# Kernel tuning notes

Measured on AMD Instinct MI355X. Metric: run time of the kernel, lower is better.

Reference implementation:

```python
import jax, jax.numpy as jnp
import numpy as np

IN_F = 4096
OUT_F = 4096
NNZ = 1638400
TOKENS = 8192


def setup_inputs() -> dict:
    key = jax.random.key(0)
    k1, k2, k3, k4, k5 = jax.random.split(key, 5)
    x = jax.random.normal(k1, (TOKENS, IN_F), dtype=jnp.float32)
    weight_pruned = jax.random.normal(k2, (NNZ,), dtype=jnp.float32)
    bias = jax.random.normal(k3, (OUT_F,), dtype=jnp.float32)
    row_idx = jax.random.randint(k4, (NNZ,), 0, OUT_F, dtype=jnp.int32)
    col_idx = jax.random.randint(k5, (NNZ,), 0, IN_F, dtype=jnp.int32)
    return {"x": x, "weight_pruned": weight_pruned, "bias": bias,
            "row_idx": row_idx, "col_idx": col_idx}


def reference(x, weight_pruned, bias, row_idx, col_idx):
    # matching torch advanced-index assignment), then dense linear.
    W = jnp.zeros((OUT_F, IN_F), dtype=weight_pruned.dtype)
    W = W.at[row_idx, col_idx].set(weight_pruned)
    return x @ W.T + bias
```

## Files before the change

### kernel.cpp

```cpp
#include <hip/hip_runtime.h>
#include <hip/hip_bf16.h>
#include <cstdint>

#define TOKENS 8192
#define IN_F 4096
#define OUT_F 4096

typedef __bf16 bf16x8 __attribute__((ext_vector_type(8)));
typedef float f32x4 __attribute__((ext_vector_type(4)));

__global__ void scatter_max_kernel(const int* __restrict__ row,
                                   const int* __restrict__ col,
                                   int* __restrict__ M, int nnz) {
    int i = blockIdx.x * blockDim.x + threadIdx.x;
    if (i < nnz) {
        atomicMax(&M[(size_t)row[i] * IN_F + col[i]], i);
    }
}

__global__ void extract_convert_kernel(const int* __restrict__ M,
                                       const float* __restrict__ w,
                                       __bf16* __restrict__ Wb,
                                       const float* __restrict__ x,
                                       __bf16* __restrict__ xb,
                                       int eb) {
    if ((int)blockIdx.x < eb) {
        size_t base = ((size_t)blockIdx.x * 256 + threadIdx.x) * 8;
        int4 m0 = *(const int4*)(M + base);
        int4 m1 = *(const int4*)(M + base + 4);
        int idx[8] = {m0.x, m0.y, m0.z, m0.w, m1.x, m1.y, m1.z, m1.w};
        bf16x8 o;
#pragma unroll
        for (int j = 0; j < 8; ++j) {
            o[j] = (idx[j] >= 0) ? (__bf16)w[idx[j]] : (__bf16)0.0f;
        }
        *(bf16x8*)(Wb + base) = o;
    } else {
        size_t base = ((size_t)(blockIdx.x - eb) * 256 + threadIdx.x) * 8;
        float4 v0 = *(const float4*)(x + base);
        float4 v1 = *(const float4*)(x + base + 4);
        bf16x8 o;
        o[0] = (__bf16)v0.x; o[1] = (__bf16)v0.y;
        o[2] = (__bf16)v0.z; o[3] = (__bf16)v0.w;
        o[4] = (__bf16)v1.x; o[5] = (__bf16)v1.y;
        o[6] = (__bf16)v1.z; o[7] = (__bf16)v1.w;
        *(bf16x8*)(xb + base) = o;
    }
}

#define BK 64
#define NT (IN_F / BK)

__global__ __launch_bounds__(512, 2) void gemm256_kernel(
    const __bf16* __restrict__ A,
    const __bf16* __restrict__ B,
    const float* __restrict__ bias,
    float* __restrict__ C) {
    extern __shared__ __bf16 sm[];

    const int tid = threadIdx.x;
    const int l   = tid & 63;
    const int wid = tid >> 6;
    const int wm  = wid >> 2;
    const int wn  = wid & 3;

    const int bid = blockIdx.y * 16 + blockIdx.x;
    const int swz = (bid & 7) * 64 + (bid >> 3);
    const int n0 = (swz & 15) * 256;
    const int m0 = (swz >> 4) * 256;

    const int srow   = tid >> 3;
    const int schunk = (tid & 7) ^ (srow & 7);
    const __bf16* gA = A + (size_t)(m0 + srow) * IN_F + schunk * 8;
    const __bf16* gB = B + (size_t)(n0 + srow) * IN_F + schunk * 8;
    const int ldsw = wid * 512;

#define GLD(SRC, LEL)                                                          \
    __builtin_amdgcn_global_load_lds(                                          \
        (unsigned int __attribute__((address_space(1)))*)(SRC),                \
        (unsigned int __attribute__((address_space(3)))*)(sm + (LEL)), 16, 0, 0);

#define STAGE_A(BUF, KT) {                                                     \
    GLD(gA + (KT),              (BUF)*16384 + 0     + ldsw)                    \
    GLD(gA + 64*IN_F  + (KT),   (BUF)*16384 + 4096  + ldsw)                    \
    GLD(gA + 128*IN_F + (KT),   (BUF)*16384 + 8192  + ldsw)                    \
    GLD(gA + 192*IN_F + (KT),   (BUF)*16384 + 12288 + ldsw) }

#define STAGE_B(BUF, KT) {                                                     \
    GLD(gB + (KT),              32768 + (BUF)*16384 + 0     + ldsw)            \
    GLD(gB + 64*IN_F  + (KT),   32768 + (BUF)*16384 + 4096  + ldsw)            \
    GLD(gB + 128*IN_F + (KT),   32768 + (BUF)*16384 + 8192  + ldsw)            \
    GLD(gB + 192*IN_F + (KT),   32768 + (BUF)*16384 + 12288 + ldsw) }

    const int g    = l >> 4;
    const int fr   = l & 15;
    const int ch0  = g ^ (l & 7);
    const int ch1  = ch0 ^ 4;
    const int arow = (wm * 128 + fr) * 64;
    const int brow = (wn * 64 + fr) * 64;

    f32x4 acc[8][4] = {};
    bf16x8 a[4][2], b[2][2];

#define LDA_H(BUF, MH) {                                                                  \
    _Pragma("unroll") for (int mf = 0; mf < 4; ++mf) {                                    \
        a[mf][0] = *(const bf16x8*)(sm + (BUF)*16384 + (MH)*4096 + arow + mf*1024 + ch0*8); \
        a[mf][1] = *(const bf16x8*)(sm + (BUF)*16384 + (MH)*4096 + arow + mf*1024 + ch1*8); } }

#define LDB_P(BUF, NB) {                                                                  \
    _Pragma("unroll") for (int j = 0; j < 2; ++j) {                                       \
        b[j][0] = *(const bf16x8*)(sm + 32768 + (BUF)*16384 + brow + ((NB)+j)*1024 + ch0*8); \
        b[j][1] = *(const bf16x8*)(sm + 32768 + (BUF)*16384 + brow + ((NB)+j)*1024 + ch1*8); } }

#define MMA(MH, NB) {                                                          \
    __builtin_amdgcn_s_setprio(1);                                             \
    _Pragma("unroll") for (int mf = 0; mf < 4; ++mf)                           \
    _Pragma("unroll") for (int j = 0; j < 2; ++j) {                            \
        acc[(MH)*4+mf][(NB)+j] = __builtin_amdgcn_mfma_f32_16x16x32_bf16(      \
            a[mf][0], b[j][0], acc[(MH)*4+mf][(NB)+j], 0, 0, 0);               \
        acc[(MH)*4+mf][(NB)+j] = __builtin_amdgcn_mfma_f32_16x16x32_bf16(      \
            a[mf][1], b[j][1], acc[(MH)*4+mf][(NB)+j], 0, 0, 0); }             \
    __builtin_amdgcn_s_setprio(0); }

#define BARRIER() { asm volatile("" ::: "memory");                             \
                    __builtin_amdgcn_s_barrier();                              \
                    asm volatile("" ::: "memory"); }
#define LGKM0()   asm volatile("s_waitcnt lgkmcnt(0)" ::: "memory");
#define VMC(N)    asm volatile("s_waitcnt vmcnt(" #N ")" ::: "memory");

    STAGE_A(0, 0)
    STAGE_B(0, 0)
    STAGE_A(1, BK)
    VMC(4)
    BARRIER()

#pragma unroll 1
    for (int t = 0; t < NT; t += 2) {
        const int k1 = (t + 1) * BK;
        const int k2 = ((t + 2) & (NT - 1)) * BK;
        const int k3 = ((t + 3) & (NT - 1)) * BK;

        LDA_H(0, 0) LDB_P(0, 0) STAGE_B(1, k1)
        BARRIER() LGKM0() MMA(0, 0) BARRIER()
        LDB_P(0, 2)
        BARRIER() LGKM0() MMA(0, 2) BARRIER()
        LDA_H(0, 1)
        BARRIER() LGKM0() MMA(1, 2) BARRIER()
        LDB_P(0, 0) STAGE_A(0, k2)
        BARRIER() LGKM0() MMA(1, 0) VMC(4) BARRIER()

        LDA_H(1, 0) LDB_P(1, 0) STAGE_B(0, k2)
        BARRIER() LGKM0() MMA(0, 0) BARRIER()
        LDB_P(1, 2)
        BARRIER() LGKM0() MMA(0, 2) BARRIER()
        LDA_H(1, 1)
        BARRIER() LGKM0() MMA(1, 2) BARRIER()
        LDB_P(1, 0) STAGE_A(1, k3)
        BARRIER() LGKM0() MMA(1, 0) VMC(4) BARRIER()
    }
    VMC(0)

    float bv[4];
#pragma unroll
    for (int nf = 0; nf < 4; ++nf) bv[nf] = bias[n0 + wn * 64 + nf * 16 + fr];
    const int r0 = m0 + wm * 128 + g * 4;
#pragma unroll
    for (int mh = 0; mh < 2; ++mh)
#pragma unroll
        for (int mf = 0; mf < 4; ++mf)
#pragma unroll
            for (int nf = 0; nf < 4; ++nf) {
                const int col = n0 + wn * 64 + nf * 16 + fr;
#pragma unroll
                for (int i = 0; i < 4; ++i)
                    C[(size_t)(r0 + mh * 64 + mf * 16 + i) * OUT_F + col] =
                        acc[mh * 4 + mf][nf][i] + bv[nf];
            }
}

extern "C" void kernel_launch(void* const* d_in, const int* in_sizes, int n_in,
                              void* d_out, int out_size, void* d_ws, size_t ws_size,
                              hipStream_t stream) {
    const float* x    = (const float*)d_in[0];
    const float* w    = (const float*)d_in[1];
    const float* bias = (const float*)d_in[2];
    const int*   row  = (const int*)d_in[3];
    const int*   col  = (const int*)d_in[4];
    float* out = (float*)d_out;
    const int nnz = in_sizes[3];

    __bf16* xb = (__bf16*)d_ws;
    __bf16* Wb = (__bf16*)((char*)d_ws + (size_t)TOKENS * IN_F * 2);
    int* M = (int*)d_out;

    static bool attr_done = false;
    if (!attr_done) {
        hipFuncSetAttribute(reinterpret_cast<const void*>(gemm256_kernel),
                            hipFuncAttributeMaxDynamicSharedMemorySize, 131072);
        attr_done = true;
    }

    hipMemsetAsync(M, 0xFF, (size_t)OUT_F * IN_F * 4, stream);

    scatter_max_kernel<<<(nnz + 255) / 256, 256, 0, stream>>>(row, col, M, nnz);

    const int eb = OUT_F * IN_F / (256 * 8);
    const int cb = TOKENS * IN_F / (256 * 8);
    extract_convert_kernel<<<eb + cb, 256, 0, stream>>>(M, w, Wb, x, xb, eb);

    dim3 grid(OUT_F / 256, TOKENS / 256);
    gemm256_kernel<<<grid, 512, 131072, stream>>>(xb, Wb, bias, out);
}
```

Baseline: 567.2 us.

## Software-pipeline LDS fragment loads across MFMA phases with partial lgkm waits

Restructures the GEMM main loop so LDS fragment loads for the next phase (and the next k-tile) are issued before the current MFMA block. Each phase then waits with lgkmcnt(6) instead of fully draining, and the extra barrier pairs are gone. Separate double-buffered register sets (aP/aQ, b01E/b01O, b23) carry fragments across phases, and global stage loads are rescheduled with a single vmcnt(0) per tile. Launch bounds drop to one block per CU to make room for the extra registers, giving up occupancy in exchange for overlapping LDS reads with matrix work.

```diff
diff --git a/kernel.cpp b/kernel.cpp
--- a/kernel.cpp
+++ b/kernel.cpp
@@ -51,7 +51,7 @@
 #define BK 64
 #define NT (IN_F / BK)
 
-__global__ __launch_bounds__(512, 2) void gemm256_kernel(
+__global__ __launch_bounds__(512, 1) void gemm256_kernel(
     const __bf16* __restrict__ A,
     const __bf16* __restrict__ B,
     const float* __restrict__ bias,
@@ -100,65 +100,71 @@
     const int brow = (wn * 64 + fr) * 64;
 
     f32x4 acc[8][4] = {};
-    bf16x8 a[4][2], b[2][2];
-
-#define LDA_H(BUF, MH) {                                                                  \
-    _Pragma("unroll") for (int mf = 0; mf < 4; ++mf) {                                    \
-        a[mf][0] = *(const bf16x8*)(sm + (BUF)*16384 + (MH)*4096 + arow + mf*1024 + ch0*8); \
-        a[mf][1] = *(const bf16x8*)(sm + (BUF)*16384 + (MH)*4096 + arow + mf*1024 + ch1*8); } }
-
-#define LDB_P(BUF, NB) {                                                                  \
-    _Pragma("unroll") for (int j = 0; j < 2; ++j) {                                       \
-        b[j][0] = *(const bf16x8*)(sm + 32768 + (BUF)*16384 + brow + ((NB)+j)*1024 + ch0*8); \
-        b[j][1] = *(const bf16x8*)(sm + 32768 + (BUF)*16384 + brow + ((NB)+j)*1024 + ch1*8); } }
-
-#define MMA(MH, NB) {                                                          \
+    bf16x8 aP[4][2], aQ[4][2], b01E[2][2], b01O[2][2], b23[2][2];
+
+#define LDAF(DST, MF, BUF, MH) {                                                             \
+    DST[MF][0] = *(const bf16x8*)(sm + (BUF)*16384 + (MH)*4096 + arow + (MF)*1024 + ch0*8);  \
+    DST[MF][1] = *(const bf16x8*)(sm + (BUF)*16384 + (MH)*4096 + arow + (MF)*1024 + ch1*8); }
+
+#define LDBF(DST, J, BUF, NB) {                                                                    \
+    DST[J][0] = *(const bf16x8*)(sm + 32768 + (BUF)*16384 + brow + ((NB)+(J))*1024 + ch0*8);       \
+    DST[J][1] = *(const bf16x8*)(sm + 32768 + (BUF)*16384 + brow + ((NB)+(J))*1024 + ch1*8); }
+
+#define MMAC(AR, BR, MB, NB) {                                                 \
     __builtin_amdgcn_s_setprio(1);                                             \
     _Pragma("unroll") for (int mf = 0; mf < 4; ++mf)                           \
     _Pragma("unroll") for (int j = 0; j < 2; ++j) {                            \
-        acc[(MH)*4+mf][(NB)+j] = __builtin_amdgcn_mfma_f32_16x16x32_bf16(      \
-            a[mf][0], b[j][0], acc[(MH)*4+mf][(NB)+j], 0, 0, 0);               \
-        acc[(MH)*4+mf][(NB)+j] = __builtin_amdgcn_mfma_f32_16x16x32_bf16(      \
-            a[mf][1], b[j][1], acc[(MH)*4+mf][(NB)+j], 0, 0, 0); }             \
+        acc[(MB)+mf][(NB)+j] = __builtin_amdgcn_mfma_f32_16x16x32_bf16(        \
+            AR[mf][0], BR[j][0], acc[(MB)+mf][(NB)+j], 0, 0, 0);               \
+        acc[(MB)+mf][(NB)+j] = __builtin_amdgcn_mfma_f32_16x16x32_bf16(        \
+            AR[mf][1], BR[j][1], acc[(MB)+mf][(NB)+j], 0, 0, 0); }             \
     __builtin_amdgcn_s_setprio(0); }
 
-#define BARRIER() { asm volatile("" ::: "memory");                             \
+#define PEND() { asm volatile("s_waitcnt lgkmcnt(6)" ::: "memory");            \
+                 __builtin_amdgcn_s_barrier();                                 \
+                 asm volatile("" ::: "memory"); }
+#define PEND_VM() { asm volatile("s_waitcnt lgkmcnt(6) vmcnt(0)" ::: "memory");\
                     __builtin_amdgcn_s_barrier();                              \
                     asm volatile("" ::: "memory"); }
-#define LGKM0()   asm volatile("s_waitcnt lgkmcnt(0)" ::: "memory");
-#define VMC(N)    asm volatile("s_waitcnt vmcnt(" #N ")" ::: "memory");
+
+#define TILE(BUF, OBUF, BC, BN, KS) {                                          \
+                                                                       \
+    LDBF(b23, 0, BUF, 2) LDBF(b23, 1, BUF, 2) LDAF(aQ, 0, BUF, 1)              \
+    MMAC(aP, BC, 0, 0)                                                         \
+    PEND()                                                                     \
+                                                                       \
+    LDAF(aQ, 1, BUF, 1) LDAF(aQ, 2, BUF, 1) LDAF(aQ, 3, BUF, 1)                \
+    MMAC(aP, b23, 0, 2)                                                        \
+    PEND_VM()                                                                  \
+                                                                       \
+    STAGE_B(BUF, KS)                                                           \
+    LDAF(aP, 0, OBUF, 0) LDAF(aP, 1, OBUF, 0) LDBF(BN, 0, OBUF, 0)             \
+    MMAC(aQ, b23, 4, 2)                                                        \
+    PEND()                                                                     \
+                                                                       \
+    STAGE_A(BUF, KS)                                                           \
+    LDAF(aP, 2, OBUF, 0) LDAF(aP, 3, OBUF, 0) LDBF(BN, 1, OBUF, 0)             \
+    MMAC(aQ, BC, 4, 0)                                                         \
+    PEND() }
 
     STAGE_A(0, 0)
     STAGE_B(0, 0)
+    STAGE_B(1, BK)
     STAGE_A(1, BK)
-    VMC(4)
-    BARRIER()
+    asm volatile("s_waitcnt vmcnt(8)" ::: "memory");
+    __builtin_amdgcn_s_barrier();
+    asm volatile("" ::: "memory");
+    LDAF(aP, 0, 0, 0) LDAF(aP, 1, 0, 0) LDAF(aP, 2, 0, 0) LDAF(aP, 3, 0, 0)
+    LDBF(b01E, 0, 0, 0) LDBF(b01E, 1, 0, 0)
 
 #pragma unroll 1
     for (int t = 0; t < NT; t += 2) {
-        const int k1 = (t + 1) * BK;
         const int k2 = ((t + 2) & (NT - 1)) * BK;
         const int k3 = ((t + 3) & (NT - 1)) * BK;
-
-        LDA_H(0, 0) LDB_P(0, 0) STAGE_B(1, k1)
-        BARRIER() LGKM0() MMA(0, 0) BARRIER()
-        LDB_P(0, 2)
-        BARRIER() LGKM0() MMA(0, 2) BARRIER()
-        LDA_H(0, 1)
-        BARRIER() LGKM0() MMA(1, 2) BARRIER()
-        LDB_P(0, 0) STAGE_A(0, k2)
-        BARRIER() LGKM0() MMA(1, 0) VMC(4) BARRIER()
-
-        LDA_H(1, 0) LDB_P(1, 0) STAGE_B(0, k2)
-        BARRIER() LGKM0() MMA(0, 0) BARRIER()
-        LDB_P(1, 2)
-        BARRIER() LGKM0() MMA(0, 2) BARRIER()
-        LDA_H(1, 1)
-        BARRIER() LGKM0() MMA(1, 2) BARRIER()
-        LDB_P(1, 0) STAGE_A(1, k3)
-        BARRIER() LGKM0() MMA(1, 0) VMC(4) BARRIER()
-    }
-    VMC(0)
+        TILE(0, 1, b01E, b01O, k2)
+        TILE(1, 0, b01O, b01E, k3)
+    }
+    asm volatile("s_waitcnt vmcnt(0) lgkmcnt(0)" ::: "memory");
 
     float bv[4];
 #pragma unroll
```

After: 542.8 us. -4.3%, faster.
